# Kernel optimization log

Measured on AMD Instinct MI355X. Metric: run time of the kernel, lower is better.

The kernel has to match this reference:

```python
import jax, jax.numpy as jnp
import numpy as np

DIM = 256
WIN = (2, 7, 7)
NH = 8
BW = 2048  # num_windows * batch
N_TOK = WIN[0] * WIN[1] * WIN[2]  # 98


def _rel_coords_table():
    # Swin-V2 continuous log-spaced relative coordinates table, flattened to [T, 3]
    d = np.arange(-(WIN[0] - 1), WIN[0], dtype=np.float32)
    h = np.arange(-(WIN[1] - 1), WIN[1], dtype=np.float32)
    w = np.arange(-(WIN[2] - 1), WIN[2], dtype=np.float32)
    g = np.stack(np.meshgrid(d, h, w, indexing='ij'), axis=-1)  # [2Wd-1, 2Wh-1, 2Ww-1, 3]
    eps = 1e-6
    g[..., 0] /= WIN[0] - (1 - eps)
    g[..., 1] /= WIN[1] - (1 - eps)
    g[..., 2] /= WIN[2] - (1 - eps)
    g *= 8.0
    g = np.sign(g) * np.log2(np.abs(g) + 1.0) / np.log2(8.0)
    return g.reshape(-1, 3).astype(np.float32)


def _rel_pos_index():
    # integer relative position index [N, N] into the flattened table
    coords = np.stack(np.meshgrid(np.arange(WIN[0]), np.arange(WIN[1]), np.arange(WIN[2]), indexing='ij'))
    cf = coords.reshape(3, -1)
    rc = (cf[:, :, None] - cf[:, None, :]).transpose(1, 2, 0)
    rc[..., 0] += WIN[0] - 1
    rc[..., 1] += WIN[1] - 1
    rc[..., 2] += WIN[2] - 1
    rc[..., 0] *= (2 * WIN[1] - 1) * (2 * WIN[2] - 1)
    rc[..., 1] *= 2 * WIN[2] - 1
    return rc.sum(-1).astype(np.int32)  # [N, N]


def setup_inputs() -> dict:
    key = jax.random.key(0)
    ks = jax.random.split(key, 6)
    x = jax.random.normal(ks[0], (BW, N_TOK, DIM), dtype=jnp.float32)
    qkv_w = jax.random.normal(ks[1], (3 * DIM, DIM), dtype=jnp.float32) * 0.02
    q_bias = jnp.zeros((DIM,), dtype=jnp.float32)
    v_bias = jnp.zeros((DIM,), dtype=jnp.float32)
    logit_scale = jnp.log(10.0) * jnp.ones((NH, 1, 1), dtype=jnp.float32)
    cpb_w1 = jax.random.normal(ks[2], (512, 3), dtype=jnp.float32) * 0.02
    cpb_b1 = jnp.zeros((512,), dtype=jnp.float32)
    cpb_w2 = jax.random.normal(ks[3], (NH, 512), dtype=jnp.float32) * 0.02
    proj_w = jax.random.normal(ks[4], (DIM, DIM), dtype=jnp.float32) * 0.02
    proj_b = jnp.zeros((DIM,), dtype=jnp.float32)
    return {"x": x, "qkv_w": qkv_w, "q_bias": q_bias, "v_bias": v_bias,
            "logit_scale": logit_scale, "cpb_w1": cpb_w1, "cpb_b1": cpb_b1,
            "cpb_w2": cpb_w2, "proj_w": proj_w, "proj_b": proj_b}


def reference(x, qkv_w, q_bias, v_bias, logit_scale, cpb_w1, cpb_b1, cpb_w2, proj_w, proj_b):
    B_, N, C = x.shape
    hd = C // NH
    # qkv with separate q/v biases and zero k bias (Swin-V2)
    bias = jnp.concatenate([q_bias, jnp.zeros_like(q_bias), v_bias])
    qkv = (x @ qkv_w.T + bias).reshape(B_, N, 3, NH, hd).transpose(2, 0, 3, 1, 4)
    q, k, v = qkv[0], qkv[1], qkv[2]  # each [B_, NH, N, hd]
    # cosine attention: L2-normalize q, k (F.normalize eps=1e-12)
    qn = q / jnp.maximum(jnp.linalg.norm(q, axis=-1, keepdims=True), 1e-12)
    kn = k / jnp.maximum(jnp.linalg.norm(k, axis=-1, keepdims=True), 1e-12)
    attn = jnp.einsum('bhnd,bhmd->bhnm', qn, kn)
    scale = jnp.exp(jnp.minimum(logit_scale, jnp.log(jnp.float32(100.0))))  # clamp at log(1/0.01)
    attn = attn * scale  # [NH,1,1] broadcasts
    # continuous relative position bias via cpb MLP
    table = jnp.asarray(_rel_coords_table())                     # [T, 3]
    bt = jax.nn.relu(table @ cpb_w1.T + cpb_b1) @ cpb_w2.T       # [T, NH]
    idx = jnp.asarray(_rel_pos_index().reshape(-1))              # [N*N]
    rpb = bt[idx].reshape(N, N, NH).transpose(2, 0, 1)           # [NH, N, N]
    rpb = 16.0 * jax.nn.sigmoid(rpb)
    attn = jax.nn.softmax(attn + rpb[None], axis=-1)
    out = jnp.einsum('bhnm,bhmd->bhnd', attn, v).transpose(0, 2, 1, 3).reshape(B_, N, C)
    return out @ proj_w.T + proj_b
```

## Files before the change

### kernel.cpp

```cpp
#include <hip/hip_runtime.h>
#include <math.h>

typedef _Float16 f16;
typedef _Float16 f16x4 __attribute__((ext_vector_type(4)));
typedef _Float16 f16x8 __attribute__((ext_vector_type(8)));
typedef float f32x4 __attribute__((ext_vector_type(4)));

#define NTOK 98
#define BWIN 2048

#define OFF_BT    0u
#define OFF_RPB   (1u<<20)
#define OFF_WQKV  (2u<<20)
#define OFF_WPROJ (3u<<20)
#define OFF_Q     (4u<<20)
#define QKV_SZ    (2048u*8u*98u*32u*2u)
#define OFF_K     (OFF_Q + QKV_SZ)
#define OFF_V     (OFF_K + QKV_SZ)
#define OFF_AV    (OFF_V + QKV_SZ)

__device__ __forceinline__ void gload16(const f16* g, f16* l) {
  __builtin_amdgcn_global_load_lds(
      (const __attribute__((address_space(1))) void*)g,
      (__attribute__((address_space(3))) void*)l, 16, 0, 0);
}
__device__ __forceinline__ void gload16f(const float* g, float* l) {
  __builtin_amdgcn_global_load_lds(
      (const __attribute__((address_space(1))) void*)g,
      (__attribute__((address_space(3))) void*)l, 16, 0, 0);
}

__global__ void prep_bt(const float* __restrict__ w1, const float* __restrict__ b1,
                        const float* __restrict__ w2, float* __restrict__ bt) {
  int t = blockIdx.x;
  int lane = threadIdx.x;
  int a = t / 169, rem = t % 169, b = rem / 13, c = rem % 13;
  float g0 = ((float)(a - 1) / 1.000001f) * 8.0f;
  float g1 = ((float)(b - 6) / 6.000001f) * 8.0f;
  float g2 = ((float)(c - 6) / 6.000001f) * 8.0f;
  float t0 = log2f(fabsf(g0) + 1.0f) / 3.0f; t0 = (g0 < 0.f) ? -t0 : t0;
  float t1 = log2f(fabsf(g1) + 1.0f) / 3.0f; t1 = (g1 < 0.f) ? -t1 : t1;
  float t2 = log2f(fabsf(g2) + 1.0f) / 3.0f; t2 = (g2 < 0.f) ? -t2 : t2;
  float part[8] = {0.f,0.f,0.f,0.f,0.f,0.f,0.f,0.f};
#pragma unroll
  for (int jj = 0; jj < 8; jj++) {
    int j = lane * 8 + jj;
    float hv = t0 * w1[j*3] + t1 * w1[j*3+1] + t2 * w1[j*3+2] + b1[j];
    hv = fmaxf(hv, 0.f);
#pragma unroll
    for (int h = 0; h < 8; h++) part[h] += hv * w2[h*512 + j];
  }
#pragma unroll
  for (int m = 1; m < 64; m <<= 1)
#pragma unroll
    for (int h = 0; h < 8; h++) part[h] += __shfl_xor(part[h], m);
  if (lane == 0)
#pragma unroll
    for (int h = 0; h < 8; h++) bt[t*8 + h] = part[h];
}

__global__ void prep_rpb(const float* __restrict__ bt, float* __restrict__ rpb) {
  int bid = blockIdx.x;
  int h = bid / 98, i = bid % 98;
  int j = threadIdx.x;
  if (j >= 112) return;
  float v = 0.f;
  if (j < 98) {
    int di = i / 49, hi = (i % 49) / 7, wi = i % 7;
    int dj = j / 49, hj = (j % 49) / 7, wj = j % 7;
    int idx = (di - dj + 1) * 169 + (hi - hj + 6) * 13 + (wi - wj + 6);
    float t = bt[idx*8 + h];
    v = 16.0f / (1.0f + expf(-t));
  }
  rpb[(h*98 + i)*112 + j] = v;
}

__global__ void prep_wt(const float* __restrict__ qkv_w, const float* __restrict__ proj_w,
                        f16* __restrict__ wq, f16* __restrict__ wp) {
  int t = blockIdx.x * 256 + threadIdx.x;
  wq[t] = (f16)qkv_w[t];
  if (t < 256*256) wp[t] = (f16)proj_w[t];
}

__global__ __launch_bounds__(256) void qkv_gemm(
    const float* __restrict__ x, const f16* __restrict__ wq,
    const float* __restrict__ q_bias, const float* __restrict__ v_bias,
    f16* __restrict__ qw, f16* __restrict__ kw, f16* __restrict__ vw) {
  __shared__ float Alf[128*32];
  __shared__ f16 Bl[128*32];
  int tid = threadIdx.x;
  int w = tid >> 6, lane = tid & 63, q4 = lane >> 4, l15 = lane & 15;

  int bid = blockIdx.x;
  int sid = (bid & 7) * 1176 + (bid >> 3);
  int n_t = sid % 6, m_t = sid / 6;
  int m0 = m_t * 128, n0 = n_t * 128;

  f32x4 acc[2][8] = {};
  for (int ks = 0; ks < 8; ks++) {
    __syncthreads();
#pragma unroll
    for (int p = 0; p < 4; p++) {
      int e0 = p*256 + (w << 6);
      int e  = e0 + lane;
      int r  = e >> 3, kc = e & 7;
      int kc2 = kc ^ ((r & 3) << 1);
      gload16f(x + (size_t)(m0 + r)*256 + ks*32 + kc2*4, &Alf[e0*4]);
    }
#pragma unroll
    for (int p = 0; p < 2; p++) {
      int e0 = p*256 + (w << 6);
      int e  = e0 + lane;
      int r  = e >> 2, kc = e & 3;
      gload16(wq + (size_t)(n0 + r)*256 + ks*32 + kc*8, &Bl[e0*8]);
    }
    __syncthreads();
    f16x8 af[2], bf[8];
#pragma unroll
    for (int mt = 0; mt < 2; mt++) {
      int row = w*32 + mt*16 + l15;
      int co = ((q4 ^ (row & 3)) << 3);
      f32x4 a0 = *(const f32x4*)(&Alf[row*32 + co]);
      f32x4 a1 = *(const f32x4*)(&Alf[row*32 + co + 4]);
      f16x8 v;
      v[0]=(f16)a0[0]; v[1]=(f16)a0[1]; v[2]=(f16)a0[2]; v[3]=(f16)a0[3];
      v[4]=(f16)a1[0]; v[5]=(f16)a1[1]; v[6]=(f16)a1[2]; v[7]=(f16)a1[3];
      af[mt] = v;
    }
#pragma unroll
    for (int nt = 0; nt < 8; nt++)
      bf[nt] = *(const f16x8*)(&Bl[(nt*16 + l15)*32 + q4*8]);
#pragma unroll
    for (int mt = 0; mt < 2; mt++)
#pragma unroll
      for (int nt = 0; nt < 8; nt++)
        acc[mt][nt] = __builtin_amdgcn_mfma_f32_16x16x32_f16(af[mt], bf[nt], acc[mt][nt], 0, 0, 0);
  }

  int s = n_t >> 1;
  f16* dst = (s == 0) ? qw : ((s == 1) ? kw : vw);
#pragma unroll
  for (int mt = 0; mt < 2; mt++)
#pragma unroll
    for (int nt = 0; nt < 8; nt++) {
      int c = n0 + nt*16 + l15;
      int hcol = (c >> 5) & 7, d = c & 31;
      float bias = (s == 0) ? q_bias[c & 255] : ((s == 2) ? v_bias[c & 255] : 0.0f);
#pragma unroll
      for (int r = 0; r < 4; r++) {
        int m = m0 + w*32 + mt*16 + q4*4 + r;
        int b = m / 98, tok = m % 98;
        dst[((size_t)(b*8 + hcol)*98 + tok)*32 + d] = (f16)(acc[mt][nt][r] + bias);
      }
    }
}

#define P_STR 136
__global__ __launch_bounds__(256) void attn_kernel(
    const f16* __restrict__ qw, const f16* __restrict__ kw, const f16* __restrict__ vw,
    const float* __restrict__ rpb, const float* __restrict__ logit_scale,
    f16* __restrict__ av) {
  __shared__ f16 Ps[4*16*P_STR];

  int tid = threadIdx.x;
  int wv = tid >> 6, lane = tid & 63, q4 = lane >> 4, l15 = lane & 15;
  int pair = blockIdx.x * 4 + wv;
  int b = pair >> 3, h = pair & 7;
  float scale = __expf(fminf(logit_scale[h], 4.6051701859880914f));
  const f16* qg = qw + ((size_t)pair) * (98*32);
  const f16* kg = kw + ((size_t)pair) * (98*32);
  const f16* vg = vw + ((size_t)pair) * (98*32);
  f16* pbuf = &Ps[wv * 16 * P_STR];

  {
    int r = lane >> 2, c0 = 112 + (lane & 3) * 4;
    *(ushort4*)(&pbuf[r*P_STR + c0]) = ushort4{0,0,0,0};
  }

  f16x8 kf[7];
#pragma unroll
  for (int nt = 0; nt < 7; nt++) {
    int row = nt*16 + l15; if (row > 97) row = 97;
    f16x8 raw = *(const f16x8*)(kg + row*32 + q4*8);
    float ss = 0.f;
#pragma unroll
    for (int j = 0; j < 8; j++) { float v = (float)raw[j]; ss = fmaf(v, v, ss); }
    ss += __shfl_xor(ss, 16);
    ss += __shfl_xor(ss, 32);
    float inv = 1.0f / fmaxf(sqrtf(ss), 1e-12f);
#pragma unroll
    for (int j = 0; j < 8; j++) kf[nt][j] = (f16)((float)raw[j] * inv);
  }

  f16x8 vf[2][4];
#pragma unroll
  for (int n = 0; n < 2; n++)
#pragma unroll
    for (int kt = 0; kt < 4; kt++)
#pragma unroll
      for (int j = 0; j < 8; j++) {
        int tok = kt*32 + q4*8 + j; if (tok > 97) tok = 97;
        vf[n][kt][j] = vg[tok*32 + n*16 + l15];
      }

  const float* rpb_h = rpb + (size_t)h * 98 * 112;

  for (int mt = 0; mt < 7; mt++) {
    int qrow = mt*16 + l15;
    int qcl = (qrow > 97) ? 97 : qrow;
    bool qv = qrow < 98;
    f16x8 qraw = *(const f16x8*)(qg + qcl*32 + q4*8);
    float ss = 0.f;
#pragma unroll
    for (int j = 0; j < 8; j++) { float v = (float)qraw[j]; ss = fmaf(v, v, ss); }
    ss += __shfl_xor(ss, 16);
    ss += __shfl_xor(ss, 32);
    float qinv = 1.0f / fmaxf(sqrtf(ss), 1e-12f);
    f16x8 aq;
#pragma unroll
    for (int j = 0; j < 8; j++) aq[j] = (f16)((float)qraw[j] * qinv);

    f32x4 lg[7];
    __builtin_amdgcn_s_setprio(1);
#pragma unroll
    for (int nt = 0; nt < 7; nt++) {
      f32x4 z = {0.f,0.f,0.f,0.f};
      lg[nt] = __builtin_amdgcn_mfma_f32_16x16x32_f16(kf[nt], aq, z, 0, 0, 0);
    }
    __builtin_amdgcn_s_setprio(0);

    float mrow = -1e30f;
#pragma unroll
    for (int nt = 0; nt < 7; nt++) {
      float4 rp = *(const float4*)(rpb_h + (size_t)qcl*112 + nt*16 + q4*4);
#pragma unroll
      for (int r = 0; r < 4; r++) {
        int k = nt*16 + q4*4 + r;
        float rv = (r == 0) ? rp.x : (r == 1) ? rp.y : (r == 2) ? rp.z : rp.w;
        float lv = (qv && k < 98) ? fmaf(scale, lg[nt][r], rv) : -1e30f;
        lg[nt][r] = lv;
        mrow = fmaxf(mrow, lv);
      }
    }
    mrow = fmaxf(mrow, __shfl_xor(mrow, 16));
    mrow = fmaxf(mrow, __shfl_xor(mrow, 32));
    float s = 0.f;
#pragma unroll
    for (int nt = 0; nt < 7; nt++)
#pragma unroll
      for (int r = 0; r < 4; r++) {
        float p = __expf(lg[nt][r] - mrow);
        lg[nt][r] = p;
        s += p;
      }
    s += __shfl_xor(s, 16);
    s += __shfl_xor(s, 32);
    float inv = 1.0f / s;
#pragma unroll
    for (int nt = 0; nt < 7; nt++) {
      f16x4 pv;
#pragma unroll
      for (int r = 0; r < 4; r++) pv[r] = (f16)(lg[nt][r] * inv);
      *(f16x4*)(&pbuf[l15*P_STR + nt*16 + q4*4]) = pv;
    }
    f16x8 pf[4];
#pragma unroll
    for (int kt = 0; kt < 4; kt++)
      pf[kt] = *(const f16x8*)(&pbuf[l15*P_STR + kt*32 + q4*8]);
    __builtin_amdgcn_s_setprio(1);
    f32x4 oacc[2];
#pragma unroll
    for (int n = 0; n < 2; n++) {
      f32x4 acc = {0.f,0.f,0.f,0.f};
#pragma unroll
      for (int kt = 0; kt < 4; kt++)
        acc = __builtin_amdgcn_mfma_f32_16x16x32_f16(pf[kt], vf[n][kt], acc, 0, 0, 0);
      oacc[n] = acc;
    }
    __builtin_amdgcn_s_setprio(0);
#pragma unroll
    for (int n = 0; n < 2; n++) {
      int d = n*16 + l15;
#pragma unroll
      for (int r = 0; r < 4; r++) {
        int row = mt*16 + q4*4 + r;
        if (row < 98)
          av[((size_t)(b*98 + row))*256 + h*32 + d] = (f16)oacc[n][r];
      }
    }
  }
}

__global__ __launch_bounds__(256) void proj_gemm(
    const f16* __restrict__ avi, const f16* __restrict__ wp,
    const float* __restrict__ pb, float* __restrict__ out) {
  __shared__ f16 Al[128*32];
  __shared__ f16 Bl[128*32];
  int tid = threadIdx.x;
  int w = tid >> 6, lane = tid & 63, q4 = lane >> 4, l15 = lane & 15;

  int bid = blockIdx.x;
  int sid = (bid & 7) * 392 + (bid >> 3);
  int n_t = sid & 1, m_t = sid >> 1;
  int m0 = m_t * 128, n0 = n_t * 128;

  f32x4 acc[2][8] = {};
  for (int ks = 0; ks < 8; ks++) {
    __syncthreads();
#pragma unroll
    for (int p = 0; p < 2; p++) {
      int e0 = p*256 + (w << 6);
      int e  = e0 + lane;
      int r  = e >> 2, kc = e & 3;
      gload16(avi + (size_t)(m0 + r)*256 + ks*32 + kc*8, &Al[e0*8]);
      gload16(wp  + (size_t)(n0 + r)*256 + ks*32 + kc*8, &Bl[e0*8]);
    }
    __syncthreads();
    f16x8 af[2], bf[8];
#pragma unroll
    for (int mt = 0; mt < 2; mt++)
      af[mt] = *(const f16x8*)(&Al[(w*32 + mt*16 + l15)*32 + q4*8]);
#pragma unroll
    for (int nt = 0; nt < 8; nt++)
      bf[nt] = *(const f16x8*)(&Bl[(nt*16 + l15)*32 + q4*8]);
#pragma unroll
    for (int mt = 0; mt < 2; mt++)
#pragma unroll
      for (int nt = 0; nt < 8; nt++)
        acc[mt][nt] = __builtin_amdgcn_mfma_f32_16x16x32_f16(af[mt], bf[nt], acc[mt][nt], 0, 0, 0);
  }

#pragma unroll
  for (int mt = 0; mt < 2; mt++)
#pragma unroll
    for (int nt = 0; nt < 8; nt++) {
      int c = n0 + nt*16 + l15;
      float bias = pb[c];
#pragma unroll
      for (int r = 0; r < 4; r++) {
        int m = m0 + w*32 + mt*16 + q4*4 + r;
        out[(size_t)m*256 + c] = acc[mt][nt][r] + bias;
      }
    }
}

extern "C" void kernel_launch(void* const* d_in, const int* in_sizes, int n_in,
                              void* d_out, int out_size, void* d_ws, size_t ws_size,
                              hipStream_t stream) {
  const float* x           = (const float*)d_in[0];
  const float* qkv_w       = (const float*)d_in[1];
  const float* q_bias      = (const float*)d_in[2];
  const float* v_bias      = (const float*)d_in[3];
  const float* logit_scale = (const float*)d_in[4];
  const float* cpb_w1      = (const float*)d_in[5];
  const float* cpb_b1      = (const float*)d_in[6];
  const float* cpb_w2      = (const float*)d_in[7];
  const float* proj_w      = (const float*)d_in[8];
  const float* proj_b      = (const float*)d_in[9];
  char* ws = (char*)d_ws;
  float* bt  = (float*)(ws + OFF_BT);
  float* rpb = (float*)(ws + OFF_RPB);
  f16* wq    = (f16*)(ws + OFF_WQKV);
  f16* wp    = (f16*)(ws + OFF_WPROJ);
  f16* qws   = (f16*)(ws + OFF_Q);
  f16* kws   = (f16*)(ws + OFF_K);
  f16* vws   = (f16*)(ws + OFF_V);
  f16* avs   = (f16*)(ws + OFF_AV);
  float* out = (float*)d_out;

  prep_bt<<<dim3(507), dim3(64), 0, stream>>>(cpb_w1, cpb_b1, cpb_w2, bt);
  prep_rpb<<<dim3(784), dim3(128), 0, stream>>>(bt, rpb);
  prep_wt<<<dim3(768), dim3(256), 0, stream>>>(qkv_w, proj_w, wq, wp);
  qkv_gemm<<<dim3(9408), dim3(256), 0, stream>>>(x, wq, q_bias, v_bias, qws, kws, vws);
  attn_kernel<<<dim3(4096), dim3(256), 0, stream>>>(qws, kws, vws, rpb, logit_scale, avs);
  proj_gemm<<<dim3(3136), dim3(256), 0, stream>>>(avs, wp, proj_b, out);
}
```

Baseline: 778.4 us.

## Double-buffer LDS tiles in QKV and projection GEMMs to overlap loads

```diff
diff --git a/kernel.cpp b/kernel.cpp
--- a/kernel.cpp
+++ b/kernel.cpp
@@ -86,8 +86,10 @@
     const float* __restrict__ x, const f16* __restrict__ wq,
     const float* __restrict__ q_bias, const float* __restrict__ v_bias,
     f16* __restrict__ qw, f16* __restrict__ kw, f16* __restrict__ vw) {
-  __shared__ float Alf[128*32];
-  __shared__ f16 Bl[128*32];
+  __shared__ float Af0[128*32];
+  __shared__ float Af1[128*32];
+  __shared__ f16   Bf0[128*32];
+  __shared__ f16   Bf1[128*32];
   int tid = threadIdx.x;
   int w = tid >> 6, lane = tid & 63, q4 = lane >> 4, l15 = lane & 15;
 
@@ -97,45 +99,63 @@
   int m0 = m_t * 128, n0 = n_t * 128;
 
   f32x4 acc[2][8] = {};
-  for (int ks = 0; ks < 8; ks++) {
+
+#define QSTAGE(AB, BB, KS)                                                     \
+  {                                                                            \
+    _Pragma("unroll")                                                          \
+    for (int p = 0; p < 4; p++) {                                              \
+      int e0 = p*256 + (w << 6);                                               \
+      int e  = e0 + lane;                                                      \
+      int r  = e >> 3, kc = e & 7;                                             \
+      int kc2 = kc ^ ((r & 3) << 1);                                           \
+      gload16f(x + (size_t)(m0 + r)*256 + (KS)*32 + kc2*4, &AB[e0*4]);         \
+    }                                                                          \
+    _Pragma("unroll")                                                          \
+    for (int p = 0; p < 2; p++) {                                              \
+      int e0 = p*256 + (w << 6);                                               \
+      int e  = e0 + lane;                                                      \
+      int r  = e >> 2, kc = e & 3;                                             \
+      gload16(wq + (size_t)(n0 + r)*256 + (KS)*32 + kc*8, &BB[e0*8]);          \
+    }                                                                          \
+  }
+
+#define QCOMPUTE(AB, BB)                                                       \
+  {                                                                            \
+    f16x8 af[2], bf[8];                                                        \
+    _Pragma("unroll")                                                          \
+    for (int mt = 0; mt < 2; mt++) {                                           \
+      int row = w*32 + mt*16 + l15;                                            \
+      int co = ((q4 ^ (row & 3)) << 3);                                        \
+      f32x4 a0 = *(const f32x4*)(&AB[row*32 + co]);                            \
+      f32x4 a1 = *(const f32x4*)(&AB[row*32 + co + 4]);                        \
+      f16x8 v;                                                                 \
+      v[0]=(f16)a0[0]; v[1]=(f16)a0[1]; v[2]=(f16)a0[2]; v[3]=(f16)a0[3];      \
+      v[4]=(f16)a1[0]; v[5]=(f16)a1[1]; v[6]=(f16)a1[2]; v[7]=(f16)a1[3];      \
+      af[mt] = v;                                                              \
+    }                                                                          \
+    _Pragma("unroll")                                                          \
+    for (int nt = 0; nt < 8; nt++)                                             \
+      bf[nt] = *(const f16x8*)(&BB[(nt*16 + l15)*32 + q4*8]);                  \
+    _Pragma("unroll")                                                          \
+    for (int mt = 0; mt < 2; mt++)                                             \
+      _Pragma("unroll")                                                        \
+      for (int nt = 0; nt < 8; nt++)                                           \
+        acc[mt][nt] = __builtin_amdgcn_mfma_f32_16x16x32_f16(af[mt], bf[nt], acc[mt][nt], 0, 0, 0); \
+  }
+
+  QSTAGE(Af0, Bf0, 0)
+  __syncthreads();
+#pragma unroll
+  for (int ks = 0; ks < 8; ks += 2) {
+    QSTAGE(Af1, Bf1, ks + 1)
+    QCOMPUTE(Af0, Bf0)
     __syncthreads();
-#pragma unroll
-    for (int p = 0; p < 4; p++) {
-      int e0 = p*256 + (w << 6);
-      int e  = e0 + lane;
-      int r  = e >> 3, kc = e & 7;
-      int kc2 = kc ^ ((r & 3) << 1);
-      gload16f(x + (size_t)(m0 + r)*256 + ks*32 + kc2*4, &Alf[e0*4]);
-    }
-#pragma unroll
-    for (int p = 0; p < 2; p++) {
-      int e0 = p*256 + (w << 6);
-      int e  = e0 + lane;
-      int r  = e >> 2, kc = e & 3;
-      gload16(wq + (size_t)(n0 + r)*256 + ks*32 + kc*8, &Bl[e0*8]);
-    }
+    if (ks + 2 < 8) QSTAGE(Af0, Bf0, ks + 2)
+    QCOMPUTE(Af1, Bf1)
     __syncthreads();
-    f16x8 af[2], bf[8];
-#pragma unroll
-    for (int mt = 0; mt < 2; mt++) {
-      int row = w*32 + mt*16 + l15;
-      int co = ((q4 ^ (row & 3)) << 3);
-      f32x4 a0 = *(const f32x4*)(&Alf[row*32 + co]);
-      f32x4 a1 = *(const f32x4*)(&Alf[row*32 + co + 4]);
-      f16x8 v;
-      v[0]=(f16)a0[0]; v[1]=(f16)a0[1]; v[2]=(f16)a0[2]; v[3]=(f16)a0[3];
-      v[4]=(f16)a1[0]; v[5]=(f16)a1[1]; v[6]=(f16)a1[2]; v[7]=(f16)a1[3];
-      af[mt] = v;
-    }
-#pragma unroll
-    for (int nt = 0; nt < 8; nt++)
-      bf[nt] = *(const f16x8*)(&Bl[(nt*16 + l15)*32 + q4*8]);
-#pragma unroll
-    for (int mt = 0; mt < 2; mt++)
-#pragma unroll
-      for (int nt = 0; nt < 8; nt++)
-        acc[mt][nt] = __builtin_amdgcn_mfma_f32_16x16x32_f16(af[mt], bf[nt], acc[mt][nt], 0, 0, 0);
-  }
+  }
+#undef QSTAGE
+#undef QCOMPUTE
 
   int s = n_t >> 1;
   f16* dst = (s == 0) ? qw : ((s == 1) ? kw : vw);
@@ -294,8 +314,10 @@
 __global__ __launch_bounds__(256) void proj_gemm(
     const f16* __restrict__ avi, const f16* __restrict__ wp,
     const float* __restrict__ pb, float* __restrict__ out) {
-  __shared__ f16 Al[128*32];
-  __shared__ f16 Bl[128*32];
+  __shared__ f16 Ap0[128*32];
+  __shared__ f16 Ap1[128*32];
+  __shared__ f16 Bp0[128*32];
+  __shared__ f16 Bp1[128*32];
   int tid = threadIdx.x;
   int w = tid >> 6, lane = tid & 63, q4 = lane >> 4, l15 = lane & 15;
 
@@ -305,30 +327,48 @@
   int m0 = m_t * 128, n0 = n_t * 128;
 
   f32x4 acc[2][8] = {};
-  for (int ks = 0; ks < 8; ks++) {
+
+#define PSTAGE(AB, BB, KS)                                                     \
+  {                                                                            \
+    _Pragma("unroll")                                                          \
+    for (int p = 0; p < 2; p++) {                                              \
+      int e0 = p*256 + (w << 6);                                               \
+      int e  = e0 + lane;                                                      \
+      int r  = e >> 2, kc = e & 3;                                             \
+      gload16(avi + (size_t)(m0 + r)*256 + (KS)*32 + kc*8, &AB[e0*8]);         \
+      gload16(wp  + (size_t)(n0 + r)*256 + (KS)*32 + kc*8, &BB[e0*8]);         \
+    }                                                                          \
+  }
+
+#define PCOMPUTE(AB, BB)                                                       \
+  {                                                                            \
+    f16x8 af[2], bf[8];                                                        \
+    _Pragma("unroll")                                                          \
+    for (int mt = 0; mt < 2; mt++)                                             \
+      af[mt] = *(const f16x8*)(&AB[(w*32 + mt*16 + l15)*32 + q4*8]);           \
+    _Pragma("unroll")                                                          \
+    for (int nt = 0; nt < 8; nt++)                                             \
+      bf[nt] = *(const f16x8*)(&BB[(nt*16 + l15)*32 + q4*8]);                  \
+    _Pragma("unroll")                                                          \
+    for (int mt = 0; mt < 2; mt++)                                             \
+      _Pragma("unroll")                                                        \
+      for (int nt = 0; nt < 8; nt++)                                           \
+        acc[mt][nt] = __builtin_amdgcn_mfma_f32_16x16x32_f16(af[mt], bf[nt], acc[mt][nt], 0, 0, 0); \
+  }
+
+  PSTAGE(Ap0, Bp0, 0)
+  __syncthreads();
+#pragma unroll
+  for (int ks = 0; ks < 8; ks += 2) {
+    PSTAGE(Ap1, Bp1, ks + 1)
+    PCOMPUTE(Ap0, Bp0)
     __syncthreads();
-#pragma unroll
-    for (int p = 0; p < 2; p++) {
-      int e0 = p*256 + (w << 6);
-      int e  = e0 + lane;
-      int r  = e >> 2, kc = e & 3;
-      gload16(avi + (size_t)(m0 + r)*256 + ks*32 + kc*8, &Al[e0*8]);
-      gload16(wp  + (size_t)(n0 + r)*256 + ks*32 + kc*8, &Bl[e0*8]);
-    }
+    if (ks + 2 < 8) PSTAGE(Ap0, Bp0, ks + 2)
+    PCOMPUTE(Ap1, Bp1)
     __syncthreads();
-    f16x8 af[2], bf[8];
-#pragma unroll
-    for (int mt = 0; mt < 2; mt++)
-      af[mt] = *(const f16x8*)(&Al[(w*32 + mt*16 + l15)*32 + q4*8]);
-#pragma unroll
-    for (int nt = 0; nt < 8; nt++)
-      bf[nt] = *(const f16x8*)(&Bl[(nt*16 + l15)*32 + q4*8]);
-#pragma unroll
-    for (int mt = 0; mt < 2; mt++)
-#pragma unroll
-      for (int nt = 0; nt < 8; nt++)
-        acc[mt][nt] = __builtin_amdgcn_mfma_f32_16x16x32_f16(af[mt], bf[nt], acc[mt][nt], 0, 0, 0);
-  }
+  }
+#undef PSTAGE
+#undef PCOMPUTE
 
 #pragma unroll
   for (int mt = 0; mt < 2; mt++)
```

After: 781.1 us. No clear change (+0.3%).
